# Kernel tuning notes

Hardware: AMD Instinct MI355X
Metric: run time of the kernel (lower is better)

The kernel has to match this reference:

```python
import jax, jax.numpy as jnp
import numpy as np

HIDDEN_DIM = 1024
NUM_HEADS = 16
HEAD_DIM = HIDDEN_DIM // NUM_HEADS
ROPE_BASE = 10000.0


def setup_inputs() -> dict:
    key = jax.random.key(0)
    kx, kq, kk, kv, ko = jax.random.split(key, 5)
    B, S = 2, 2048
    scale = 1.0 / np.sqrt(HIDDEN_DIM)
    x = jax.random.normal(kx, (B, S, HIDDEN_DIM), dtype=jnp.float32)
    Wq = jax.random.normal(kq, (HIDDEN_DIM, HIDDEN_DIM), dtype=jnp.float32) * scale
    Wk = jax.random.normal(kk, (HIDDEN_DIM, HIDDEN_DIM), dtype=jnp.float32) * scale
    Wv = jax.random.normal(kv, (HIDDEN_DIM, HIDDEN_DIM), dtype=jnp.float32) * scale
    Wo = jax.random.normal(ko, (HIDDEN_DIM, HIDDEN_DIM), dtype=jnp.float32) * scale
    return {"x": x, "Wq": Wq, "Wk": Wk, "Wv": Wv, "Wo": Wo}


def _apply_rope(t, positions):
    # t: (B, S, H, D), positions: (B, S)
    half = HEAD_DIM // 2
    inv_freq = 1.0 / (ROPE_BASE ** (jnp.arange(0, half, dtype=jnp.float32) * 2.0 / HEAD_DIM))
    freqs = positions[..., None].astype(jnp.float32) * inv_freq  # (B, S, D/2)
    emb = jnp.concatenate([freqs, freqs], axis=-1)  # (B, S, D)
    cos = jnp.cos(emb)[:, :, None, :]
    sin = jnp.sin(emb)[:, :, None, :]
    t1, t2 = t[..., :half], t[..., half:]
    rot = jnp.concatenate([-t2, t1], axis=-1)
    return t * cos + rot * sin


def reference(x, Wq, Wk, Wv, Wo):
    B, S, _ = x.shape
    H, D = NUM_HEADS, HEAD_DIM
    q = (x @ Wq.T).reshape(B, S, H, D)
    k = (x @ Wk.T).reshape(B, S, H, D)
    v = (x @ Wv.T).reshape(B, S, H, D)
    positions = jnp.broadcast_to(jnp.arange(S)[None, :], (B, S))
    q = _apply_rope(q, positions)
    k = _apply_rope(k, positions)
    # SDPA (non-causal, no mask): scores (B, H, S, S)
    scale = 1.0 / np.sqrt(D)
    scores = jnp.einsum('bqhd,bkhd->bhqk', q, k) * scale
    probs = jax.nn.softmax(scores, axis=-1)
    out = jnp.einsum('bhqk,bkhd->bqhd', probs, v).reshape(B, S, H * D)
    return out @ Wo.T
```

## Files before the change

kernel.cpp:

```cpp
#include <hip/hip_runtime.h>


typedef unsigned short u16;
typedef __bf16 bf16x8 __attribute__((ext_vector_type(8)));
typedef float  f32x4  __attribute__((ext_vector_type(4)));
typedef u16    u16x8  __attribute__((ext_vector_type(8)));
typedef u16    u16x4  __attribute__((ext_vector_type(4)));

#define HID 1024
#define SEQ 2048
#define NH  16
#define HD  64

__device__ __forceinline__ float bf2f(u16 u) { return __uint_as_float(((unsigned)u) << 16); }
__device__ __forceinline__ u16 f2bf(float f) {
  unsigned u = __float_as_uint(f);
  u += 0x7fffu + ((u >> 16) & 1u);
  return (u16)(u >> 16);
}
__device__ __forceinline__ void gl_lds16(const void* g, void* l) {
  __builtin_amdgcn_global_load_lds((const __attribute__((address_space(1))) void*)g,
                                   (__attribute__((address_space(3))) void*)l, 16, 0, 0);
}
__device__ __forceinline__ void stage_f32(const float* __restrict__ src, u16* dst) {
  float4 f0 = *(const float4*)src;
  float4 f1 = *(const float4*)(src + 4);
  u16x8 o;
  o[0] = f2bf(f0.x); o[1] = f2bf(f0.y); o[2] = f2bf(f0.z); o[3] = f2bf(f0.w);
  o[4] = f2bf(f1.x); o[5] = f2bf(f1.y); o[6] = f2bf(f1.z); o[7] = f2bf(f1.w);
  *(u16x8*)dst = o;
}
__device__ __forceinline__ int swz(int c, int r) { return c ^ (r & 7); }

__global__ void cvt_pre(const float* __restrict__ x,  const float* __restrict__ Wq,
                        const float* __restrict__ Wk, const float* __restrict__ Wv,
                        u16* __restrict__ xb, u16* __restrict__ Wqb,
                        u16* __restrict__ Wkb, u16* __restrict__ Wvb) {
  const int z = blockIdx.y;
  const float* src; u16* dst; int nchunk;
  switch (z) {
    case 0:  src = x;  dst = xb;  nchunk = 524288; break;
    case 1:  src = Wq; dst = Wqb; nchunk = 131072; break;
    case 2:  src = Wk; dst = Wkb; nchunk = 131072; break;
    default: src = Wv; dst = Wvb; nchunk = 131072; break;
  }
  const int i = blockIdx.x * 256 + threadIdx.x;
  if (i >= nchunk) return;
  stage_f32(src + (size_t)i * 8, dst + (size_t)i * 8);
}
__global__ void cvt_wo(const float* __restrict__ Wo, u16* __restrict__ Wob) {
  const int i = blockIdx.x * 256 + threadIdx.x;
  stage_f32(Wo + (size_t)i * 8, Wob + (size_t)i * 8);
}

__device__ __forceinline__ void gemm_mainloop(const u16* __restrict__ Aptr,
                                              const u16* __restrict__ Bptr,
                                              u16* a_lds, u16* b_lds,
                                              int m0, int n0, f32x4 (&acc)[4][4]) {
  const int tid  = threadIdx.x;
  const int w    = tid >> 6;
  const int lane = tid & 63;
  const int quad = lane >> 4, l15 = lane & 15;
  const int wm = (w >> 1) * 64, wn = (w & 1) * 64;
  const int srow = lane >> 3, sc = lane & 7;

  for (int k0 = 0; k0 < HID; k0 += 64) {
#pragma unroll
    for (int i = 0; i < 4; ++i) {
      const int seg = w * 4 + i;
      const int r   = seg * 8 + srow;
      const int col = k0 + swz(sc, srow) * 8;
      gl_lds16(Aptr + (size_t)(m0 + r) * HID + col, a_lds + seg * 512);
      gl_lds16(Bptr + (size_t)(n0 + r) * HID + col, b_lds + seg * 512);
    }
    __syncthreads();
#pragma unroll
    for (int kf = 0; kf < 2; ++kf) {
      bf16x8 af[4], bfr[4];
#pragma unroll
      for (int mt = 0; mt < 4; ++mt)
        af[mt] = *(const bf16x8*)&a_lds[(wm + mt * 16 + l15) * 64 + swz(kf * 4 + quad, l15) * 8];
#pragma unroll
      for (int nt = 0; nt < 4; ++nt)
        bfr[nt] = *(const bf16x8*)&b_lds[(wn + nt * 16 + l15) * 64 + swz(kf * 4 + quad, l15) * 8];
#pragma unroll
      for (int mt = 0; mt < 4; ++mt)
#pragma unroll
        for (int nt = 0; nt < 4; ++nt)
          acc[mt][nt] = __builtin_amdgcn_mfma_f32_16x16x32_bf16(af[mt], bfr[nt], acc[mt][nt], 0, 0, 0);
    }
    __syncthreads();
  }
}

__global__ __launch_bounds__(256, 2) void qkv_gemm(const u16* __restrict__ xb,
                                                   const u16* __restrict__ Wqb,
                                                   const u16* __restrict__ Wkb,
                                                   const u16* __restrict__ Wvb,
                                                   u16* __restrict__ q, u16* __restrict__ k,
                                                   u16* __restrict__ vT) {
  __shared__ __align__(16) u16 a_lds[128 * 64];
  __shared__ __align__(16) u16 b_lds[128 * 64];
  const int z = blockIdx.z;
  const u16* W = (z == 0) ? Wqb : (z == 1) ? Wkb : Wvb;

  f32x4 acc[4][4];
#pragma unroll
  for (int i = 0; i < 4; ++i)
#pragma unroll
    for (int j = 0; j < 4; ++j) acc[i][j] = (f32x4){0.f, 0.f, 0.f, 0.f};

  const int m0 = blockIdx.y * 128, n0 = blockIdx.x * 128;
  gemm_mainloop(xb, W, a_lds, b_lds, m0, n0, acc);

  const int tid = threadIdx.x, w = tid >> 6, lane = tid & 63;
  const int quad = lane >> 4, l15 = lane & 15;
  const int wm = (w >> 1) * 64, wn = (w & 1) * 64;

  if (z != 2) {
    float fr[2];
    fr[0] = __expf(-(float)(l15)      * 0.2878231366242557f);
    fr[1] = __expf(-(float)(16 + l15) * 0.2878231366242557f);
    const float qs = (z == 0) ? 0.125f : 1.f;
#pragma unroll
    for (int mt = 0; mt < 4; ++mt)
#pragma unroll
      for (int r = 0; r < 4; ++r) {
        const int s = (m0 + wm + mt * 16 + quad * 4 + r) & 2047;
#pragma unroll
        for (int p = 0; p < 2; ++p) {
          float c, sn;
          __sincosf((float)s * fr[p], &sn, &c);
          const float t1 = acc[mt][p][r], t2 = acc[mt][p + 2][r];
          acc[mt][p][r]     = (t1 * c - t2 * sn) * qs;
          acc[mt][p + 2][r] = (t2 * c + t1 * sn) * qs;
        }
      }
    u16* dst = (z == 0) ? q : k;
#pragma unroll
    for (int mt = 0; mt < 4; ++mt)
#pragma unroll
      for (int nt = 0; nt < 4; ++nt) {
        const int col = n0 + wn + nt * 16 + l15;
        const int h = col >> 6, d = col & 63;
#pragma unroll
        for (int r = 0; r < 4; ++r) {
          const int row = m0 + wm + mt * 16 + quad * 4 + r;
          const int bh  = (row >> 11) * NH + h;
          dst[((size_t)bh * SEQ + (row & 2047)) * HD + d] = f2bf(acc[mt][nt][r]);
        }
      }
  } else {
#pragma unroll
    for (int mt = 0; mt < 4; ++mt) {
      const int rowbase = m0 + wm + mt * 16 + quad * 4;
      const int b = rowbase >> 11, s0 = rowbase & 2047;
#pragma unroll
      for (int nt = 0; nt < 4; ++nt) {
        const int col = n0 + wn + nt * 16 + l15;
        const int h = col >> 6, d = col & 63;
        u16x4 o;
#pragma unroll
        for (int r = 0; r < 4; ++r) o[r] = f2bf(acc[mt][nt][r]);
        *(u16x4*)&vT[((size_t)(b * NH + h) * HD + d) * SEQ + s0] = o;
      }
    }
  }
}

__global__ __launch_bounds__(256, 3) void flash(const u16* __restrict__ q,
                                                const u16* __restrict__ k,
                                                const u16* __restrict__ vT,
                                                u16* __restrict__ o0, u16* __restrict__ o1,
                                                float* __restrict__ L0, float* __restrict__ L1) {
  __shared__ __align__(16) u16 ktl[2 * 4096];
  __shared__ __align__(16) u16 vtl[2 * 4096];
  __shared__ __align__(16) u16 pl[4 * 16 * 72];

  const int tid = threadIdx.x, w = tid >> 6, lane = tid & 63;
  const int quad = lane >> 4, l15 = lane & 15;
  const int srow = lane >> 3, sc = lane & 7;
  const int bh = blockIdx.y;
  const int q0 = blockIdx.x * 128;
  const int z  = blockIdx.z;
  u16*   odst = z ? o1 : o0;
  float* Ldst = z ? L1 : L0;

  bf16x8 qa[2][2];
#pragma unroll
  for (int qh = 0; qh < 2; ++qh) {
    const u16* qrow = q + ((size_t)bh * SEQ + q0 + w * 32 + qh * 16 + l15) * HD + quad * 8;
    qa[qh][0] = *(const bf16x8*)qrow;
    qa[qh][1] = *(const bf16x8*)(qrow + 32);
  }

  f32x4 oacc[2][4];
#pragma unroll
  for (int qh = 0; qh < 2; ++qh)
#pragma unroll
    for (int i = 0; i < 4; ++i) oacc[qh][i] = (f32x4){0.f, 0.f, 0.f, 0.f};
  float L[2] = {0.f, 0.f};

  const u16* kbase = k  + (size_t)bh * SEQ * HD + (size_t)z * 1024 * HD;
  const u16* vtb   = vT + (size_t)bh * HD * SEQ + (size_t)z * 1024;

#pragma unroll
  for (int i = 0; i < 2; ++i) {
    const int seg = w * 2 + i, r = seg * 8 + srow, col = swz(sc, srow) * 8;
    gl_lds16(kbase + (size_t)r * HD + col,  &ktl[seg * 512]);
    gl_lds16(vtb   + (size_t)r * SEQ + col, &vtl[seg * 512]);
  }
  __syncthreads();

  for (int t = 0; t < 16; ++t) {
    const int t0 = t * 64, buf = t & 1;
    if (t < 15) {
#pragma unroll
      for (int i = 0; i < 2; ++i) {
        const int seg = w * 2 + i, r = seg * 8 + srow, col = swz(sc, srow) * 8;
        gl_lds16(kbase + (size_t)(t0 + 64 + r) * HD + col, &ktl[(buf ^ 1) * 4096 + seg * 512]);
        gl_lds16(vtb   + (size_t)r * SEQ + t0 + 64 + col,  &vtl[(buf ^ 1) * 4096 + seg * 512]);
      }
    }

    bf16x8 kfr[2][4], bvf[2][4];
#pragma unroll
    for (int kf = 0; kf < 2; ++kf)
#pragma unroll
      for (int nt = 0; nt < 4; ++nt) {
        kfr[kf][nt] = *(const bf16x8*)&ktl[buf * 4096 + (nt * 16 + l15) * 64 + swz(kf * 4 + quad, l15) * 8];
        bvf[kf][nt] = *(const bf16x8*)&vtl[buf * 4096 + (nt * 16 + l15) * 64 + swz(kf * 4 + quad, l15) * 8];
      }

    u16* pw = &pl[w * 16 * 72];
#pragma unroll
    for (int qh = 0; qh < 2; ++qh) {
      f32x4 sv[4];
#pragma unroll
      for (int nt = 0; nt < 4; ++nt) {
        sv[nt] = (f32x4){0.f, 0.f, 0.f, 0.f};
#pragma unroll
        for (int kf = 0; kf < 2; ++kf)
          sv[nt] = __builtin_amdgcn_mfma_f32_16x16x32_bf16(kfr[kf][nt], qa[qh][kf], sv[nt], 0, 0, 0);
      }
#pragma unroll
      for (int nt = 0; nt < 4; ++nt) {
        u16x4 pk;
#pragma unroll
        for (int r = 0; r < 4; ++r) {
          const float pv = __expf(sv[nt][r]);
          L[qh] += pv;
          pk[r] = f2bf(pv);
        }
        *(u16x4*)&pw[l15 * 72 + nt * 16 + quad * 4] = pk;
      }
#pragma unroll
      for (int kf = 0; kf < 2; ++kf) {
        bf16x8 ap = *(const bf16x8*)&pw[l15 * 72 + kf * 32 + quad * 8];
#pragma unroll
        for (int dt = 0; dt < 4; ++dt)
          oacc[qh][dt] = __builtin_amdgcn_mfma_f32_16x16x32_bf16(ap, bvf[kf][dt], oacc[qh][dt], 0, 0, 0);
      }
    }
    __syncthreads();
  }

#pragma unroll
  for (int qh = 0; qh < 2; ++qh) {
    L[qh] += __shfl_xor(L[qh], 16, 64);
    L[qh] += __shfl_xor(L[qh], 32, 64);
    if (quad == 0) Ldst[(size_t)bh * SEQ + q0 + w * 32 + qh * 16 + l15] = L[qh];
  }

  const int b = bh >> 4, h = bh & 15;
#pragma unroll
  for (int qh = 0; qh < 2; ++qh)
#pragma unroll
    for (int r = 0; r < 4; ++r) {
      const int row = b * SEQ + q0 + w * 32 + qh * 16 + quad * 4 + r;
#pragma unroll
      for (int dt = 0; dt < 4; ++dt)
        odst[(size_t)row * HID + h * HD + dt * 16 + l15] = f2bf(oacc[qh][dt][r]);
    }
}

__global__ void combine(const u16* __restrict__ o1, const float* __restrict__ L0,
                        const float* __restrict__ L1, u16* __restrict__ attn) {
  const size_t base = ((size_t)blockIdx.x * 256 + threadIdx.x) * 8;
  const int row = (int)(base >> 10);
  const int h   = ((int)base & 1023) >> 6;
  const int bh  = (row >> 11) * NH + h;
  const int s   = row & 2047;
  const float inv = 1.f / (L0[(size_t)bh * SEQ + s] + L1[(size_t)bh * SEQ + s]);
  u16x8 a = *(const u16x8*)&attn[base];
  u16x8 b = *(const u16x8*)&o1[base];
  u16x8 o;
#pragma unroll
  for (int j = 0; j < 8; ++j) o[j] = f2bf((bf2f(a[j]) + bf2f(b[j])) * inv);
  *(u16x8*)&attn[base] = o;
}

__global__ __launch_bounds__(256, 2) void out_gemm(const u16* __restrict__ attn,
                                                   const u16* __restrict__ Wob,
                                                   float* __restrict__ out) {
  __shared__ __align__(16) u16 a_lds[64 * 64];
  __shared__ __align__(16) u16 b_lds[128 * 64];
  const int tid = threadIdx.x, w = tid >> 6, lane = tid & 63;
  const int quad = lane >> 4, l15 = lane & 15;
  const int wm = (w >> 1) * 32, wn = (w & 1) * 64;
  const int srow = lane >> 3, sc = lane & 7;

  f32x4 acc[2][4];
#pragma unroll
  for (int i = 0; i < 2; ++i)
#pragma unroll
    for (int j = 0; j < 4; ++j) acc[i][j] = (f32x4){0.f, 0.f, 0.f, 0.f};

  const int m0 = blockIdx.y * 64, n0 = blockIdx.x * 128;

  for (int k0 = 0; k0 < HID; k0 += 64) {
#pragma unroll
    for (int i = 0; i < 2; ++i) {
      const int seg = w * 2 + i, r = seg * 8 + srow;
      gl_lds16(attn + (size_t)(m0 + r) * HID + k0 + swz(sc, srow) * 8, a_lds + seg * 512);
    }
#pragma unroll
    for (int i = 0; i < 4; ++i) {
      const int seg = w * 4 + i, r = seg * 8 + srow;
      gl_lds16(Wob + (size_t)(n0 + r) * HID + k0 + swz(sc, srow) * 8, b_lds + seg * 512);
    }
    __syncthreads();
#pragma unroll
    for (int kf = 0; kf < 2; ++kf) {
      bf16x8 af[2], bfr[4];
#pragma unroll
      for (int mt = 0; mt < 2; ++mt)
        af[mt] = *(const bf16x8*)&a_lds[(wm + mt * 16 + l15) * 64 + swz(kf * 4 + quad, l15) * 8];
#pragma unroll
      for (int nt = 0; nt < 4; ++nt)
        bfr[nt] = *(const bf16x8*)&b_lds[(wn + nt * 16 + l15) * 64 + swz(kf * 4 + quad, l15) * 8];
#pragma unroll
      for (int mt = 0; mt < 2; ++mt)
#pragma unroll
        for (int nt = 0; nt < 4; ++nt)
          acc[mt][nt] = __builtin_amdgcn_mfma_f32_16x16x32_bf16(af[mt], bfr[nt], acc[mt][nt], 0, 0, 0);
    }
    __syncthreads();
  }

#pragma unroll
  for (int mt = 0; mt < 2; ++mt)
#pragma unroll
    for (int nt = 0; nt < 4; ++nt) {
      const int col = n0 + wn + nt * 16 + l15;
#pragma unroll
      for (int r = 0; r < 4; ++r) {
        const int row = m0 + wm + mt * 16 + quad * 4 + r;
        out[(size_t)row * HID + col] = acc[mt][nt][r];
      }
    }
}

extern "C" void kernel_launch(void* const* d_in, const int* in_sizes, int n_in,
                              void* d_out, int out_size, void* d_ws, size_t ws_size,
                              hipStream_t stream) {
  const float* x  = (const float*)d_in[0];
  const float* Wq = (const float*)d_in[1];
  const float* Wk = (const float*)d_in[2];
  const float* Wv = (const float*)d_in[3];
  const float* Wo = (const float*)d_in[4];
  float* out = (float*)d_out;

  char* os = (char*)d_out;
  u16* Wqb = (u16*)(os);
  u16* Wkb = (u16*)(os + (2u << 20));
  u16* Wvb = (u16*)(os + (4u << 20));
  u16* xb  = (u16*)(os + (6u << 20));
  u16*   o1 = (u16*)(os);
  float* L0 = (float*)(os + (8u << 20));
  float* L1 = (float*)(os + (8u << 20) + (256u << 10));

  char* ws = (char*)d_ws;
  u16* q    = (u16*)(ws);
  u16* Wob  = (u16*)(ws);
  u16* k    = (u16*)(ws + (8u << 20));
  u16* vT   = (u16*)(ws + (16u << 20));
  u16* attn = (u16*)(ws + (24u << 20));

  cvt_pre<<<dim3(2048, 4), 256, 0, stream>>>(x, Wq, Wk, Wv, xb, Wqb, Wkb, Wvb);
  qkv_gemm<<<dim3(8, 32, 3), 256, 0, stream>>>(xb, Wqb, Wkb, Wvb, q, k, vT);
  flash<<<dim3(16, 32, 2), 256, 0, stream>>>(q, k, vT, attn, o1, L0, L1);
  cvt_wo<<<dim3(512), 256, 0, stream>>>(Wo, Wob);
  combine<<<dim3(2048), 256, 0, stream>>>(o1, L0, L1, attn);
  out_gemm<<<dim3(8, 64), 256, 0, stream>>>(attn, Wob, out);
}
```

Before: 195.5 us.

## Shrink QKV GEMM tiles, use exp2 softmax, swizzle P tile, raise occupancy

The QKV projection now uses 64x128 tiles through a shared mainloop that out_gemm also calls, which doubles the grid and raises launch bounds to 4 blocks per CU. The Q scale now folds in log2(e) so the flash kernel can use a hardware exp2 in place of __expf. The P staging buffer drops its padding and uses an XOR swizzle to cut LDS footprint and avoid bank conflicts, and flash occupancy rises from 3 to 4. The bf16 conversion switches to the compiler's native cast. Higher occupancy bounds may force register spills, and smaller tiles reduce data reuse per block.

Result: slower. 209.9 us (+7.3%).

```diff
diff --git a/kernel.cpp b/kernel.cpp
--- a/kernel.cpp
+++ b/kernel.cpp
@@ -12,11 +12,17 @@
 #define NH  16
 #define HD  64
 
+#if __has_builtin(__builtin_amdgcn_exp2f)
+#define EXP2F(x) __builtin_amdgcn_exp2f(x)
+#else
+#define EXP2F(x) exp2f(x)
+#endif
+
 __device__ __forceinline__ float bf2f(u16 u) { return __uint_as_float(((unsigned)u) << 16); }
 __device__ __forceinline__ u16 f2bf(float f) {
-  unsigned u = __float_as_uint(f);
-  u += 0x7fffu + ((u >> 16) & 1u);
-  return (u16)(u >> 16);
+  union { __bf16 h; u16 u; } c;
+  c.h = (__bf16)f;
+  return c.u;
 }
 __device__ __forceinline__ void gl_lds16(const void* g, void* l) {
   __builtin_amdgcn_global_load_lds((const __attribute__((address_space(1))) void*)g,
@@ -53,38 +59,40 @@
   stage_f32(Wo + (size_t)i * 8, Wob + (size_t)i * 8);
 }
 
-__device__ __forceinline__ void gemm_mainloop(const u16* __restrict__ Aptr,
-                                              const u16* __restrict__ Bptr,
-                                              u16* a_lds, u16* b_lds,
-                                              int m0, int n0, f32x4 (&acc)[4][4]) {
+__device__ __forceinline__ void gemm64_mainloop(const u16* __restrict__ Aptr,
+                                                const u16* __restrict__ Bptr,
+                                                u16* a_lds, u16* b_lds,
+                                                int m0, int n0, f32x4 (&acc)[2][4]) {
   const int tid  = threadIdx.x;
   const int w    = tid >> 6;
   const int lane = tid & 63;
   const int quad = lane >> 4, l15 = lane & 15;
-  const int wm = (w >> 1) * 64, wn = (w & 1) * 64;
+  const int wm = (w >> 1) * 32, wn = (w & 1) * 64;
   const int srow = lane >> 3, sc = lane & 7;
 
   for (int k0 = 0; k0 < HID; k0 += 64) {
 #pragma unroll
+    for (int i = 0; i < 2; ++i) {
+      const int seg = w * 2 + i, r = seg * 8 + srow;
+      gl_lds16(Aptr + (size_t)(m0 + r) * HID + k0 + swz(sc, srow) * 8, a_lds + seg * 512);
+    }
+#pragma unroll
     for (int i = 0; i < 4; ++i) {
-      const int seg = w * 4 + i;
-      const int r   = seg * 8 + srow;
-      const int col = k0 + swz(sc, srow) * 8;
-      gl_lds16(Aptr + (size_t)(m0 + r) * HID + col, a_lds + seg * 512);
-      gl_lds16(Bptr + (size_t)(n0 + r) * HID + col, b_lds + seg * 512);
+      const int seg = w * 4 + i, r = seg * 8 + srow;
+      gl_lds16(Bptr + (size_t)(n0 + r) * HID + k0 + swz(sc, srow) * 8, b_lds + seg * 512);
     }
     __syncthreads();
 #pragma unroll
     for (int kf = 0; kf < 2; ++kf) {
-      bf16x8 af[4], bfr[4];
-#pragma unroll
-      for (int mt = 0; mt < 4; ++mt)
+      bf16x8 af[2], bfr[4];
+#pragma unroll
+      for (int mt = 0; mt < 2; ++mt)
         af[mt] = *(const bf16x8*)&a_lds[(wm + mt * 16 + l15) * 64 + swz(kf * 4 + quad, l15) * 8];
 #pragma unroll
       for (int nt = 0; nt < 4; ++nt)
         bfr[nt] = *(const bf16x8*)&b_lds[(wn + nt * 16 + l15) * 64 + swz(kf * 4 + quad, l15) * 8];
 #pragma unroll
-      for (int mt = 0; mt < 4; ++mt)
+      for (int mt = 0; mt < 2; ++mt)
 #pragma unroll
         for (int nt = 0; nt < 4; ++nt)
           acc[mt][nt] = __builtin_amdgcn_mfma_f32_16x16x32_bf16(af[mt], bfr[nt], acc[mt][nt], 0, 0, 0);
@@ -93,37 +101,38 @@
   }
 }
 
-__global__ __launch_bounds__(256, 2) void qkv_gemm(const u16* __restrict__ xb,
+#define QS_LOG2E 0.18033688011112042f
+__global__ __launch_bounds__(256, 4) void qkv_gemm(const u16* __restrict__ xb,
                                                    const u16* __restrict__ Wqb,
                                                    const u16* __restrict__ Wkb,
                                                    const u16* __restrict__ Wvb,
                                                    u16* __restrict__ q, u16* __restrict__ k,
                                                    u16* __restrict__ vT) {
-  __shared__ __align__(16) u16 a_lds[128 * 64];
+  __shared__ __align__(16) u16 a_lds[64 * 64];
   __shared__ __align__(16) u16 b_lds[128 * 64];
   const int z = blockIdx.z;
   const u16* W = (z == 0) ? Wqb : (z == 1) ? Wkb : Wvb;
 
-  f32x4 acc[4][4];
-#pragma unroll
-  for (int i = 0; i < 4; ++i)
+  f32x4 acc[2][4];
+#pragma unroll
+  for (int i = 0; i < 2; ++i)
 #pragma unroll
     for (int j = 0; j < 4; ++j) acc[i][j] = (f32x4){0.f, 0.f, 0.f, 0.f};
 
-  const int m0 = blockIdx.y * 128, n0 = blockIdx.x * 128;
-  gemm_mainloop(xb, W, a_lds, b_lds, m0, n0, acc);
+  const int m0 = blockIdx.y * 64, n0 = blockIdx.x * 128;
+  gemm64_mainloop(xb, W, a_lds, b_lds, m0, n0, acc);
 
   const int tid = threadIdx.x, w = tid >> 6, lane = tid & 63;
   const int quad = lane >> 4, l15 = lane & 15;
-  const int wm = (w >> 1) * 64, wn = (w & 1) * 64;
+  const int wm = (w >> 1) * 32, wn = (w & 1) * 64;
 
   if (z != 2) {
     float fr[2];
     fr[0] = __expf(-(float)(l15)      * 0.2878231366242557f);
     fr[1] = __expf(-(float)(16 + l15) * 0.2878231366242557f);
-    const float qs = (z == 0) ? 0.125f : 1.f;
-#pragma unroll
-    for (int mt = 0; mt < 4; ++mt)
+    const float qs = (z == 0) ? QS_LOG2E : 1.f;
+#pragma unroll
+    for (int mt = 0; mt < 2; ++mt)
 #pragma unroll
       for (int r = 0; r < 4; ++r) {
         const int s = (m0 + wm + mt * 16 + quad * 4 + r) & 2047;
@@ -138,7 +147,7 @@
       }
     u16* dst = (z == 0) ? q : k;
 #pragma unroll
-    for (int mt = 0; mt < 4; ++mt)
+    for (int mt = 0; mt < 2; ++mt)
 #pragma unroll
       for (int nt = 0; nt < 4; ++nt) {
         const int col = n0 + wn + nt * 16 + l15;
@@ -152,7 +161,7 @@
       }
   } else {
 #pragma unroll
-    for (int mt = 0; mt < 4; ++mt) {
+    for (int mt = 0; mt < 2; ++mt) {
       const int rowbase = m0 + wm + mt * 16 + quad * 4;
       const int b = rowbase >> 11, s0 = rowbase & 2047;
 #pragma unroll
@@ -168,14 +177,14 @@
   }
 }
 
-__global__ __launch_bounds__(256, 3) void flash(const u16* __restrict__ q,
+__global__ __launch_bounds__(256, 4) void flash(const u16* __restrict__ q,
                                                 const u16* __restrict__ k,
                                                 const u16* __restrict__ vT,
                                                 u16* __restrict__ o0, u16* __restrict__ o1,
                                                 float* __restrict__ L0, float* __restrict__ L1) {
   __shared__ __align__(16) u16 ktl[2 * 4096];
   __shared__ __align__(16) u16 vtl[2 * 4096];
-  __shared__ __align__(16) u16 pl[4 * 16 * 72];
+  __shared__ __align__(16) u16 pl[4 * 16 * 64];
 
   const int tid = threadIdx.x, w = tid >> 6, lane = tid & 63;
   const int quad = lane >> 4, l15 = lane & 15;
@@ -194,11 +203,12 @@
     qa[qh][1] = *(const bf16x8*)(qrow + 32);
   }
 
+  const f32x4 zero4 = (f32x4){0.f, 0.f, 0.f, 0.f};
   f32x4 oacc[2][4];
 #pragma unroll
   for (int qh = 0; qh < 2; ++qh)
 #pragma unroll
-    for (int i = 0; i < 4; ++i) oacc[qh][i] = (f32x4){0.f, 0.f, 0.f, 0.f};
+    for (int i = 0; i < 4; ++i) oacc[qh][i] = zero4;
   float L[2] = {0.f, 0.f};
 
   const u16* kbase = k  + (size_t)bh * SEQ * HD + (size_t)z * 1024 * HD;
@@ -232,31 +242,30 @@
         bvf[kf][nt] = *(const bf16x8*)&vtl[buf * 4096 + (nt * 16 + l15) * 64 + swz(kf * 4 + quad, l15) * 8];
       }
 
-    u16* pw = &pl[w * 16 * 72];
+    u16* pw = &pl[w * 16 * 64];
 #pragma unroll
     for (int qh = 0; qh < 2; ++qh) {
       f32x4 sv[4];
 #pragma unroll
       for (int nt = 0; nt < 4; ++nt) {
-        sv[nt] = (f32x4){0.f, 0.f, 0.f, 0.f};
-#pragma unroll
-        for (int kf = 0; kf < 2; ++kf)
-          sv[nt] = __builtin_amdgcn_mfma_f32_16x16x32_bf16(kfr[kf][nt], qa[qh][kf], sv[nt], 0, 0, 0);
+        sv[nt] = __builtin_amdgcn_mfma_f32_16x16x32_bf16(kfr[0][nt], qa[qh][0], zero4, 0, 0, 0);
+        sv[nt] = __builtin_amdgcn_mfma_f32_16x16x32_bf16(kfr[1][nt], qa[qh][1], sv[nt], 0, 0, 0);
       }
 #pragma unroll
       for (int nt = 0; nt < 4; ++nt) {
         u16x4 pk;
 #pragma unroll
         for (int r = 0; r < 4; ++r) {
-          const float pv = __expf(sv[nt][r]);
+          const float pv = EXP2F(sv[nt][r]);
           L[qh] += pv;
           pk[r] = f2bf(pv);
         }
-        *(u16x4*)&pw[l15 * 72 + nt * 16 + quad * 4] = pk;
+        const int cw = 2 * nt + (quad >> 1);
+        *(u16x4*)&pw[l15 * 64 + swz(cw, l15) * 8 + 4 * (quad & 1)] = pk;
       }
 #pragma unroll
       for (int kf = 0; kf < 2; ++kf) {
-        bf16x8 ap = *(const bf16x8*)&pw[l15 * 72 + kf * 32 + quad * 8];
+        bf16x8 ap = *(const bf16x8*)&pw[l15 * 64 + swz(kf * 4 + quad, l15) * 8];
 #pragma unroll
         for (int dt = 0; dt < 4; ++dt)
           oacc[qh][dt] = __builtin_amdgcn_mfma_f32_16x16x32_bf16(ap, bvf[kf][dt], oacc[qh][dt], 0, 0, 0);
@@ -300,54 +309,23 @@
   *(u16x8*)&attn[base] = o;
 }
 
-__global__ __launch_bounds__(256, 2) void out_gemm(const u16* __restrict__ attn,
+__global__ __launch_bounds__(256, 4) void out_gemm(const u16* __restrict__ attn,
                                                    const u16* __restrict__ Wob,
                                                    float* __restrict__ out) {
   __shared__ __align__(16) u16 a_lds[64 * 64];
   __shared__ __align__(16) u16 b_lds[128 * 64];
+  f32x4 acc[2][4];
+#pragma unroll
+  for (int i = 0; i < 2; ++i)
+#pragma unroll
+    for (int j = 0; j < 4; ++j) acc[i][j] = (f32x4){0.f, 0.f, 0.f, 0.f};
+
+  const int m0 = blockIdx.y * 64, n0 = blockIdx.x * 128;
+  gemm64_mainloop(attn, Wob, a_lds, b_lds, m0, n0, acc);
+
   const int tid = threadIdx.x, w = tid >> 6, lane = tid & 63;
   const int quad = lane >> 4, l15 = lane & 15;
   const int wm = (w >> 1) * 32, wn = (w & 1) * 64;
-  const int srow = lane >> 3, sc = lane & 7;
-
-  f32x4 acc[2][4];
-#pragma unroll
-  for (int i = 0; i < 2; ++i)
-#pragma unroll
-    for (int j = 0; j < 4; ++j) acc[i][j] = (f32x4){0.f, 0.f, 0.f, 0.f};
-
-  const int m0 = blockIdx.y * 64, n0 = blockIdx.x * 128;
-
-  for (int k0 = 0; k0 < HID; k0 += 64) {
-#pragma unroll
-    for (int i = 0; i < 2; ++i) {
-      const int seg = w * 2 + i, r = seg * 8 + srow;
-      gl_lds16(attn + (size_t)(m0 + r) * HID + k0 + swz(sc, srow) * 8, a_lds + seg * 512);
-    }
-#pragma unroll
-    for (int i = 0; i < 4; ++i) {
-      const int seg = w * 4 + i, r = seg * 8 + srow;
-      gl_lds16(Wob + (size_t)(n0 + r) * HID + k0 + swz(sc, srow) * 8, b_lds + seg * 512);
-    }
-    __syncthreads();
-#pragma unroll
-    for (int kf = 0; kf < 2; ++kf) {
-      bf16x8 af[2], bfr[4];
-#pragma unroll
-      for (int mt = 0; mt < 2; ++mt)
-        af[mt] = *(const bf16x8*)&a_lds[(wm + mt * 16 + l15) * 64 + swz(kf * 4 + quad, l15) * 8];
-#pragma unroll
-      for (int nt = 0; nt < 4; ++nt)
-        bfr[nt] = *(const bf16x8*)&b_lds[(wn + nt * 16 + l15) * 64 + swz(kf * 4 + quad, l15) * 8];
-#pragma unroll
-      for (int mt = 0; mt < 2; ++mt)
-#pragma unroll
-        for (int nt = 0; nt < 4; ++nt)
-          acc[mt][nt] = __builtin_amdgcn_mfma_f32_16x16x32_bf16(af[mt], bfr[nt], acc[mt][nt], 0, 0, 0);
-    }
-    __syncthreads();
-  }
-
 #pragma unroll
   for (int mt = 0; mt < 2; ++mt)
 #pragma unroll
@@ -388,7 +366,7 @@
   u16* attn = (u16*)(ws + (24u << 20));
 
   cvt_pre<<<dim3(2048, 4), 256, 0, stream>>>(x, Wq, Wk, Wv, xb, Wqb, Wkb, Wvb);
-  qkv_gemm<<<dim3(8, 32, 3), 256, 0, stream>>>(xb, Wqb, Wkb, Wvb, q, k, vT);
+  qkv_gemm<<<dim3(8, 64, 3), 256, 0, stream>>>(xb, Wqb, Wkb, Wvb, q, k, vT);
   flash<<<dim3(16, 32, 2), 256, 0, stream>>>(q, k, vT, attn, o1, L0, L1);
   cvt_wo<<<dim3(512), 256, 0, stream>>>(Wo, Wob);
   combine<<<dim3(2048), 256, 0, stream>>>(o1, L0, L1, attn);
```

## Double flash query tile per block, use exp2 with folded log2e, swizzle P buffer

Applied to the files above, without the earlier changes.

The flash kernel now processes 256 query rows per block (64 per wave) instead of 128, so each K/V tile loaded into LDS is reused across twice as many queries; grid x halves and launch bounds drop to 2 blocks/CU. The softmax uses the hardware exp2 with log2(e) folded into the Q scale, and the P scratch buffer switches from padded rows to an XOR swizzle. The bf16 conversion uses the native cast, and out_gemm is refactored into a shared mainloop with a higher occupancy hint. Doubling per-wave accumulators raises register pressure and lowers occupancy.

After: 179.2 us. -8.4%, faster.

```diff
diff --git a/kernel.cpp b/kernel.cpp
--- a/kernel.cpp
+++ b/kernel.cpp
@@ -12,11 +12,17 @@
 #define NH  16
 #define HD  64
 
+#if __has_builtin(__builtin_amdgcn_exp2f)
+#define EXP2F(x) __builtin_amdgcn_exp2f(x)
+#else
+#define EXP2F(x) exp2f(x)
+#endif
+
 __device__ __forceinline__ float bf2f(u16 u) { return __uint_as_float(((unsigned)u) << 16); }
 __device__ __forceinline__ u16 f2bf(float f) {
-  unsigned u = __float_as_uint(f);
-  u += 0x7fffu + ((u >> 16) & 1u);
-  return (u16)(u >> 16);
+  union { __bf16 h; u16 u; } c;
+  c.h = (__bf16)f;
+  return c.u;
 }
 __device__ __forceinline__ void gl_lds16(const void* g, void* l) {
   __builtin_amdgcn_global_load_lds((const __attribute__((address_space(1))) void*)g,
@@ -93,6 +99,49 @@
   }
 }
 
+__device__ __forceinline__ void gemm64_mainloop(const u16* __restrict__ Aptr,
+                                                const u16* __restrict__ Bptr,
+                                                u16* a_lds, u16* b_lds,
+                                                int m0, int n0, f32x4 (&acc)[2][4]) {
+  const int tid  = threadIdx.x;
+  const int w    = tid >> 6;
+  const int lane = tid & 63;
+  const int quad = lane >> 4, l15 = lane & 15;
+  const int wm = (w >> 1) * 32, wn = (w & 1) * 64;
+  const int srow = lane >> 3, sc = lane & 7;
+
+  for (int k0 = 0; k0 < HID; k0 += 64) {
+#pragma unroll
+    for (int i = 0; i < 2; ++i) {
+      const int seg = w * 2 + i, r = seg * 8 + srow;
+      gl_lds16(Aptr + (size_t)(m0 + r) * HID + k0 + swz(sc, srow) * 8, a_lds + seg * 512);
+    }
+#pragma unroll
+    for (int i = 0; i < 4; ++i) {
+      const int seg = w * 4 + i, r = seg * 8 + srow;
+      gl_lds16(Bptr + (size_t)(n0 + r) * HID + k0 + swz(sc, srow) * 8, b_lds + seg * 512);
+    }
+    __syncthreads();
+#pragma unroll
+    for (int kf = 0; kf < 2; ++kf) {
+      bf16x8 af[2], bfr[4];
+#pragma unroll
+      for (int mt = 0; mt < 2; ++mt)
+        af[mt] = *(const bf16x8*)&a_lds[(wm + mt * 16 + l15) * 64 + swz(kf * 4 + quad, l15) * 8];
+#pragma unroll
+      for (int nt = 0; nt < 4; ++nt)
+        bfr[nt] = *(const bf16x8*)&b_lds[(wn + nt * 16 + l15) * 64 + swz(kf * 4 + quad, l15) * 8];
+#pragma unroll
+      for (int mt = 0; mt < 2; ++mt)
+#pragma unroll
+        for (int nt = 0; nt < 4; ++nt)
+          acc[mt][nt] = __builtin_amdgcn_mfma_f32_16x16x32_bf16(af[mt], bfr[nt], acc[mt][nt], 0, 0, 0);
+    }
+    __syncthreads();
+  }
+}
+
+#define QS_LOG2E 0.18033688011112042f
 __global__ __launch_bounds__(256, 2) void qkv_gemm(const u16* __restrict__ xb,
                                                    const u16* __restrict__ Wqb,
                                                    const u16* __restrict__ Wkb,
@@ -121,7 +170,7 @@
     float fr[2];
     fr[0] = __expf(-(float)(l15)      * 0.2878231366242557f);
     fr[1] = __expf(-(float)(16 + l15) * 0.2878231366242557f);
-    const float qs = (z == 0) ? 0.125f : 1.f;
+    const float qs = (z == 0) ? QS_LOG2E : 1.f;
 #pragma unroll
     for (int mt = 0; mt < 4; ++mt)
 #pragma unroll
@@ -168,38 +217,39 @@
   }
 }
 
-__global__ __launch_bounds__(256, 3) void flash(const u16* __restrict__ q,
+__global__ __launch_bounds__(256, 2) void flash(const u16* __restrict__ q,
                                                 const u16* __restrict__ k,
                                                 const u16* __restrict__ vT,
                                                 u16* __restrict__ o0, u16* __restrict__ o1,
                                                 float* __restrict__ L0, float* __restrict__ L1) {
   __shared__ __align__(16) u16 ktl[2 * 4096];
   __shared__ __align__(16) u16 vtl[2 * 4096];
-  __shared__ __align__(16) u16 pl[4 * 16 * 72];
+  __shared__ __align__(16) u16 pl[4 * 16 * 64];
 
   const int tid = threadIdx.x, w = tid >> 6, lane = tid & 63;
   const int quad = lane >> 4, l15 = lane & 15;
   const int srow = lane >> 3, sc = lane & 7;
   const int bh = blockIdx.y;
-  const int q0 = blockIdx.x * 128;
+  const int q0 = blockIdx.x * 256;
   const int z  = blockIdx.z;
   u16*   odst = z ? o1 : o0;
   float* Ldst = z ? L1 : L0;
 
-  bf16x8 qa[2][2];
-#pragma unroll
-  for (int qh = 0; qh < 2; ++qh) {
-    const u16* qrow = q + ((size_t)bh * SEQ + q0 + w * 32 + qh * 16 + l15) * HD + quad * 8;
+  bf16x8 qa[4][2];
+#pragma unroll
+  for (int qh = 0; qh < 4; ++qh) {
+    const u16* qrow = q + ((size_t)bh * SEQ + q0 + w * 64 + qh * 16 + l15) * HD + quad * 8;
     qa[qh][0] = *(const bf16x8*)qrow;
     qa[qh][1] = *(const bf16x8*)(qrow + 32);
   }
 
-  f32x4 oacc[2][4];
-#pragma unroll
-  for (int qh = 0; qh < 2; ++qh)
-#pragma unroll
-    for (int i = 0; i < 4; ++i) oacc[qh][i] = (f32x4){0.f, 0.f, 0.f, 0.f};
-  float L[2] = {0.f, 0.f};
+  const f32x4 zero4 = (f32x4){0.f, 0.f, 0.f, 0.f};
+  f32x4 oacc[4][4];
+#pragma unroll
+  for (int qh = 0; qh < 4; ++qh)
+#pragma unroll
+    for (int i = 0; i < 4; ++i) oacc[qh][i] = zero4;
+  float L[4] = {0.f, 0.f, 0.f, 0.f};
 
   const u16* kbase = k  + (size_t)bh * SEQ * HD + (size_t)z * 1024 * HD;
   const u16* vtb   = vT + (size_t)bh * HD * SEQ + (size_t)z * 1024;
@@ -232,31 +282,30 @@
         bvf[kf][nt] = *(const bf16x8*)&vtl[buf * 4096 + (nt * 16 + l15) * 64 + swz(kf * 4 + quad, l15) * 8];
       }
 
-    u16* pw = &pl[w * 16 * 72];
-#pragma unroll
-    for (int qh = 0; qh < 2; ++qh) {
+    u16* pw = &pl[w * 16 * 64];
+#pragma unroll
+    for (int qh = 0; qh < 4; ++qh) {
       f32x4 sv[4];
 #pragma unroll
       for (int nt = 0; nt < 4; ++nt) {
-        sv[nt] = (f32x4){0.f, 0.f, 0.f, 0.f};
-#pragma unroll
-        for (int kf = 0; kf < 2; ++kf)
-          sv[nt] = __builtin_amdgcn_mfma_f32_16x16x32_bf16(kfr[kf][nt], qa[qh][kf], sv[nt], 0, 0, 0);
+        sv[nt] = __builtin_amdgcn_mfma_f32_16x16x32_bf16(kfr[0][nt], qa[qh][0], zero4, 0, 0, 0);
+        sv[nt] = __builtin_amdgcn_mfma_f32_16x16x32_bf16(kfr[1][nt], qa[qh][1], sv[nt], 0, 0, 0);
       }
 #pragma unroll
       for (int nt = 0; nt < 4; ++nt) {
         u16x4 pk;
 #pragma unroll
         for (int r = 0; r < 4; ++r) {
-          const float pv = __expf(sv[nt][r]);
+          const float pv = EXP2F(sv[nt][r]);
           L[qh] += pv;
           pk[r] = f2bf(pv);
         }
-        *(u16x4*)&pw[l15 * 72 + nt * 16 + quad * 4] = pk;
+        const int cw = 2 * nt + (quad >> 1);
+        *(u16x4*)&pw[l15 * 64 + swz(cw, l15) * 8 + 4 * (quad & 1)] = pk;
       }
 #pragma unroll
       for (int kf = 0; kf < 2; ++kf) {
-        bf16x8 ap = *(const bf16x8*)&pw[l15 * 72 + kf * 32 + quad * 8];
+        bf16x8 ap = *(const bf16x8*)&pw[l15 * 64 + swz(kf * 4 + quad, l15) * 8];
 #pragma unroll
         for (int dt = 0; dt < 4; ++dt)
           oacc[qh][dt] = __builtin_amdgcn_mfma_f32_16x16x32_bf16(ap, bvf[kf][dt], oacc[qh][dt], 0, 0, 0);
@@ -266,18 +315,18 @@
   }
 
 #pragma unroll
-  for (int qh = 0; qh < 2; ++qh) {
+  for (int qh = 0; qh < 4; ++qh) {
     L[qh] += __shfl_xor(L[qh], 16, 64);
     L[qh] += __shfl_xor(L[qh], 32, 64);
-    if (quad == 0) Ldst[(size_t)bh * SEQ + q0 + w * 32 + qh * 16 + l15] = L[qh];
+    if (quad == 0) Ldst[(size_t)bh * SEQ + q0 + w * 64 + qh * 16 + l15] = L[qh];
   }
 
   const int b = bh >> 4, h = bh & 15;
 #pragma unroll
-  for (int qh = 0; qh < 2; ++qh)
+  for (int qh = 0; qh < 4; ++qh)
 #pragma unroll
     for (int r = 0; r < 4; ++r) {
-      const int row = b * SEQ + q0 + w * 32 + qh * 16 + quad * 4 + r;
+      const int row = b * SEQ + q0 + w * 64 + qh * 16 + quad * 4 + r;
 #pragma unroll
       for (int dt = 0; dt < 4; ++dt)
         odst[(size_t)row * HID + h * HD + dt * 16 + l15] = f2bf(oacc[qh][dt][r]);
@@ -300,54 +349,23 @@
   *(u16x8*)&attn[base] = o;
 }
 
-__global__ __launch_bounds__(256, 2) void out_gemm(const u16* __restrict__ attn,
+__global__ __launch_bounds__(256, 4) void out_gemm(const u16* __restrict__ attn,
                                                    const u16* __restrict__ Wob,
                                                    float* __restrict__ out) {
   __shared__ __align__(16) u16 a_lds[64 * 64];
   __shared__ __align__(16) u16 b_lds[128 * 64];
+  f32x4 acc[2][4];
+#pragma unroll
+  for (int i = 0; i < 2; ++i)
+#pragma unroll
+    for (int j = 0; j < 4; ++j) acc[i][j] = (f32x4){0.f, 0.f, 0.f, 0.f};
+
+  const int m0 = blockIdx.y * 64, n0 = blockIdx.x * 128;
+  gemm64_mainloop(attn, Wob, a_lds, b_lds, m0, n0, acc);
+
   const int tid = threadIdx.x, w = tid >> 6, lane = tid & 63;
   const int quad = lane >> 4, l15 = lane & 15;
   const int wm = (w >> 1) * 32, wn = (w & 1) * 64;
-  const int srow = lane >> 3, sc = lane & 7;
-
-  f32x4 acc[2][4];
-#pragma unroll
-  for (int i = 0; i < 2; ++i)
-#pragma unroll
-    for (int j = 0; j < 4; ++j) acc[i][j] = (f32x4){0.f, 0.f, 0.f, 0.f};
-
-  const int m0 = blockIdx.y * 64, n0 = blockIdx.x * 128;
-
-  for (int k0 = 0; k0 < HID; k0 += 64) {
-#pragma unroll
-    for (int i = 0; i < 2; ++i) {
-      const int seg = w * 2 + i, r = seg * 8 + srow;
-      gl_lds16(attn + (size_t)(m0 + r) * HID + k0 + swz(sc, srow) * 8, a_lds + seg * 512);
-    }
-#pragma unroll
-    for (int i = 0; i < 4; ++i) {
-      const int seg = w * 4 + i, r = seg * 8 + srow;
-      gl_lds16(Wob + (size_t)(n0 + r) * HID + k0 + swz(sc, srow) * 8, b_lds + seg * 512);
-    }
-    __syncthreads();
-#pragma unroll
-    for (int kf = 0; kf < 2; ++kf) {
-      bf16x8 af[2], bfr[4];
-#pragma unroll
-      for (int mt = 0; mt < 2; ++mt)
-        af[mt] = *(const bf16x8*)&a_lds[(wm + mt * 16 + l15) * 64 + swz(kf * 4 + quad, l15) * 8];
-#pragma unroll
-      for (int nt = 0; nt < 4; ++nt)
-        bfr[nt] = *(const bf16x8*)&b_lds[(wn + nt * 16 + l15) * 64 + swz(kf * 4 + quad, l15) * 8];
-#pragma unroll
-      for (int mt = 0; mt < 2; ++mt)
-#pragma unroll
-        for (int nt = 0; nt < 4; ++nt)
-          acc[mt][nt] = __builtin_amdgcn_mfma_f32_16x16x32_bf16(af[mt], bfr[nt], acc[mt][nt], 0, 0, 0);
-    }
-    __syncthreads();
-  }
-
 #pragma unroll
   for (int mt = 0; mt < 2; ++mt)
 #pragma unroll
@@ -389,7 +407,7 @@
 
   cvt_pre<<<dim3(2048, 4), 256, 0, stream>>>(x, Wq, Wk, Wv, xb, Wqb, Wkb, Wvb);
   qkv_gemm<<<dim3(8, 32, 3), 256, 0, stream>>>(xb, Wqb, Wkb, Wvb, q, k, vT);
-  flash<<<dim3(16, 32, 2), 256, 0, stream>>>(q, k, vT, attn, o1, L0, L1);
+  flash<<<dim3(8, 32, 2), 256, 0, stream>>>(q, k, vT, attn, o1, L0, L1);
   cvt_wo<<<dim3(512), 256, 0, stream>>>(Wo, Wob);
   combine<<<dim3(2048), 256, 0, stream>>>(o1, L0, L1, attn);
   out_gemm<<<dim3(8, 64), 256, 0, stream>>>(attn, Wob, out);
```
